# Optimization experiments

Hardware: AMD Instinct MI355X
Metric: run time of the kernel (lower is better)

## Reference

```python
import jax, jax.numpy as jnp
import numpy as np

DIM = 2048
DIM_HEAD = 128
HEADS = 16
FF_MULT = 4
EPS = 1e-05
ATTN_INNER = DIM_HEAD * HEADS          # 2048
FF_INNER = DIM * FF_MULT               # 8192
FUSED_DIMS = (ATTN_INNER, DIM_HEAD, DIM_HEAD, FF_INNER, FF_INNER)
SPLITS = np.cumsum(FUSED_DIMS[:-1]).tolist()
RMS_SCALE = DIM ** 0.5
Q_SCALE = DIM_HEAD ** (-0.5)


def setup_inputs() -> dict:
    key = jax.random.key(0)
    k1, k2, k3, k4, k5 = jax.random.split(key, 5)
    B, S = 2, 2048
    x = jax.random.normal(k1, (B, S, DIM), dtype=jnp.float32)
    attn_bias = jax.random.normal(k2, (HEADS, S, S), dtype=jnp.float32)
    # learned params (scaled for numerical sanity; math identical to module)
    gamma = jnp.ones((DIM,), dtype=jnp.float32)
    wi = jax.random.normal(k3, (DIM, sum(FUSED_DIMS)), dtype=jnp.float32) * 0.02
    attn_wo = jax.random.normal(k4, (ATTN_INNER, DIM), dtype=jnp.float32) * 0.02
    ff_wo = jax.random.normal(k5, (FF_INNER, DIM), dtype=jnp.float32) * 0.02
    return {"x": x, "attn_bias": attn_bias, "gamma": gamma,
            "wi": wi, "attn_wo": attn_wo, "ff_wo": ff_wo}


def reference(x, attn_bias, gamma, wi, attn_wo, ff_wo):
    B, S, _ = x.shape
    # RMSNorm
    inv_norm = jax.lax.rsqrt(jnp.sum(jnp.square(x), axis=-1, keepdims=True) + EPS)
    xn = inv_norm * x * gamma * RMS_SCALE
    # fused projection
    proj = xn @ wi  # [B, S, sum(fused_dims)]
    q, k, v, ff, ff_gate = jnp.split(proj, SPLITS, axis=-1)
    # q: [B, S, H*Dh] -> [B, H, S, Dh]; k, v stay single-head [B, S, Dh] (MQA)
    q = q.reshape(B, S, HEADS, DIM_HEAD).transpose(0, 2, 1, 3) * Q_SCALE
    sim = jnp.einsum('bhid,bjd->bhij', q, k) + attn_bias  # [B, H, S, S]
    attn = jax.nn.softmax(sim, axis=-1)
    out = jnp.einsum('bhij,bjd->bhid', attn, v)  # [B, H, S, Dh]
    out = out.transpose(0, 2, 1, 3).reshape(B, S, ATTN_INNER)
    attn_out = out @ attn_wo
    ff_out = (ff * jax.nn.swish(ff_gate)) @ ff_wo
    return attn_out + ff_out
```

## Files before the change

### kernel.cpp

```cpp
#include <hip/hip_runtime.h>
#include <cstdint>

typedef unsigned short u16;
typedef short bf16x8 __attribute__((ext_vector_type(8)));
typedef float f32x4 __attribute__((ext_vector_type(4)));

#define PLD 18688
#define ALD 10240
#define LOG2E 1.4426950408889634f
#define QSCALE 0.08838834764831845f
#define RMS_SCALE 45.25483399593904f

__device__ __forceinline__ u16 f2bf(float f) {
  union { float f; unsigned int u; } v; v.f = f;
  unsigned int u = v.u;
  return (u16)((u + 0x7fffu + ((u >> 16) & 1u)) >> 16);
}
__device__ __forceinline__ float bf2f(u16 h) {
  union { unsigned int u; float f; } v; v.u = ((unsigned int)h) << 16;
  return v.f;
}

__device__ __forceinline__ void gload_lds16(const void* g, void* l) {
  __builtin_amdgcn_global_load_lds((__attribute__((address_space(1))) void*)(g),
                                   (__attribute__((address_space(3))) void*)(l),
                                   16, 0, 0);
}

__global__ __launch_bounds__(256) void rmsnorm_kernel(const float* __restrict__ x,
                                                      const float* __restrict__ gamma,
                                                      u16* __restrict__ xn) {
  const int row = blockIdx.x;
  const int tid = threadIdx.x;
  const float4* xr = (const float4*)(x + (size_t)row * 2048);
  float4 v0 = xr[tid], v1 = xr[tid + 256];
  float s = v0.x*v0.x + v0.y*v0.y + v0.z*v0.z + v0.w*v0.w
          + v1.x*v1.x + v1.y*v1.y + v1.z*v1.z + v1.w*v1.w;
  for (int m = 1; m < 64; m <<= 1) s += __shfl_xor(s, m, 64);
  __shared__ float red[4];
  if ((tid & 63) == 0) red[tid >> 6] = s;
  __syncthreads();
  float tot = red[0] + red[1] + red[2] + red[3];
  float inv = rsqrtf(tot + 1e-5f) * RMS_SCALE;
  const float4* gp = (const float4*)gamma;
  float4 g0 = gp[tid], g1 = gp[tid + 256];
  u16* xo = xn + (size_t)row * 2048;
  union { u16 h[4]; uint2 u; } o0, o1;
  o0.h[0] = f2bf(v0.x*inv*g0.x); o0.h[1] = f2bf(v0.y*inv*g0.y);
  o0.h[2] = f2bf(v0.z*inv*g0.z); o0.h[3] = f2bf(v0.w*inv*g0.w);
  o1.h[0] = f2bf(v1.x*inv*g1.x); o1.h[1] = f2bf(v1.y*inv*g1.y);
  o1.h[2] = f2bf(v1.z*inv*g1.z); o1.h[3] = f2bf(v1.w*inv*g1.w);
  *(uint2*)(xo + tid*4) = o0.u;
  *(uint2*)(xo + (tid+256)*4) = o1.u;
}

__global__ __launch_bounds__(256) void tconv(const float* __restrict__ src,
                                             u16* __restrict__ dst,
                                             int K, int N, int dstride, int doff) {
  __shared__ u16 t[32][33];
  const int tx = threadIdx.x & 31, ty = threadIdx.x >> 5;
  const int n0 = blockIdx.x * 32, k0 = blockIdx.y * 32;
  #pragma unroll
  for (int yy = 0; yy < 4; yy++) {
    int r = ty + yy*8;
    t[r][tx] = f2bf(src[(size_t)(k0 + r) * N + n0 + tx]);
  }
  __syncthreads();
  #pragma unroll
  for (int yy = 0; yy < 4; yy++) {
    int r = ty + yy*8;
    dst[(size_t)(n0 + r) * dstride + doff + k0 + tx] = t[tx][r];
  }
}

template <int OUT_BF16, int GC>
__global__ __launch_bounds__(256) void gemm_bt(const u16* __restrict__ A,
                                               const u16* __restrict__ Bt,
                                               void* __restrict__ Cv,
                                               int M, int N, int K) {
  __shared__ alignas(16) u16 sA[128*32];
  __shared__ alignas(16) u16 sB[128*32];
  const int numRow = M >> 7;
  const int per = GC * numRow;
  const int pid = blockIdx.x;
  const int g = pid / per, inner = pid % per;
  const int colT = g * GC + inner / numRow;
  const int rowT = inner % numRow;
  const int row0 = rowT * 128, col0 = colT * 128;

  const int tid = threadIdx.x;
  const int w = tid >> 6, lane = tid & 63, quad = lane >> 4, l16 = lane & 15;
  const int wr = (w >> 1) * 64, wc = (w & 1) * 64;
  const f32x4 zero = {0.f, 0.f, 0.f, 0.f};
  f32x4 acc[4][4];
  #pragma unroll
  for (int mi = 0; mi < 4; mi++)
    #pragma unroll
    for (int ni = 0; ni < 4; ni++) acc[mi][ni] = zero;

  for (int k0 = 0; k0 < K; k0 += 32) {
    __syncthreads();
    #pragma unroll
    for (int i = 0; i < 2; i++) {
      const int segbase = (i*4 + w) * 64;
      const int seg = segbase + lane;
      const int r = seg >> 2, c = (seg & 3) * 8;
      gload_lds16(A  + (size_t)(row0 + r) * K + k0 + c, sA + segbase * 8);
      gload_lds16(Bt + (size_t)(col0 + r) * K + k0 + c, sB + segbase * 8);
    }
    __syncthreads();
    bf16x8 af[4], bfr[4];
    #pragma unroll
    for (int mi = 0; mi < 4; mi++)
      af[mi] = *(const bf16x8*)&sA[(wr + mi*16 + l16)*32 + quad*8];
    #pragma unroll
    for (int ni = 0; ni < 4; ni++)
      bfr[ni] = *(const bf16x8*)&sB[(wc + ni*16 + l16)*32 + quad*8];
    #pragma unroll
    for (int mi = 0; mi < 4; mi++)
      #pragma unroll
      for (int ni = 0; ni < 4; ni++)
        acc[mi][ni] = __builtin_amdgcn_mfma_f32_16x16x32_bf16(af[mi], bfr[ni], acc[mi][ni], 0, 0, 0);
  }

  #pragma unroll
  for (int mi = 0; mi < 4; mi++) {
    const int rb = row0 + wr + mi*16 + quad*4;
    #pragma unroll
    for (int ni = 0; ni < 4; ni++) {
      const int cb = col0 + wc + ni*16 + l16;
      #pragma unroll
      for (int r = 0; r < 4; r++) {
        if (OUT_BF16) ((u16*)Cv)[(size_t)(rb + r) * N + cb] = f2bf(acc[mi][ni][r]);
        else          ((float*)Cv)[(size_t)(rb + r) * N + cb] = acc[mi][ni][r];
      }
    }
  }
}

#define BAR() do { asm volatile("" ::: "memory"); __builtin_amdgcn_s_barrier(); asm volatile("" ::: "memory"); } while (0)
#define WAITV(N) asm volatile("s_waitcnt vmcnt(" #N ")" ::: "memory")

template <int OUT_BF16>
__global__ __launch_bounds__(512, 2) void gemm256(const u16* __restrict__ A,
                                                  const u16* __restrict__ Bt,
                                                  void* __restrict__ Cv,
                                                  int M, int N, int K) {
  __shared__ alignas(16) u16 lds[65536];
  u16* const sB = lds + 32768;

  const int numRow = M >> 8;
  int pid = blockIdx.x;
  {
    const int nwg = gridDim.x;
    const int q = nwg >> 3, r = nwg & 7;
    const int xcd = pid & 7, lid = pid >> 3;
    pid = (xcd < r ? xcd * (q + 1) : r * (q + 1) + (xcd - r) * q) + lid;
  }
  const int colT = pid / numRow, rowT = pid % numRow;
  const int row0 = rowT << 8, col0 = colT << 8;

  const int tid = threadIdx.x;
  const int w = tid >> 6, lane = tid & 63, quad = lane >> 4, l16 = lane & 15;
  const int wr = w >> 2, wc = w & 3;

  const u16* aG  = A  + (size_t)(row0 + w * 16 + l16) * K + quad * 8;
  const u16* aG2 = aG + (size_t)128 * K;
  const u16* bG  = Bt + (size_t)(col0 + w * 16 + l16) * K + quad * 8;
  const u16* bG2 = bG + (size_t)128 * K;

  #define STAGE_A(bb, ks, kt) do { \
    gload_lds16(aG  + (kt) + (ks) * 32, lds + (bb) * 16384 + (ks) * 8192 + w * 512); \
    gload_lds16(aG2 + (kt) + (ks) * 32, lds + (bb) * 16384 + (ks) * 8192 + (8 + w) * 512); \
  } while (0)
  #define STAGE_B(bb, ks, kt) do { \
    gload_lds16(bG  + (kt) + (ks) * 32, sB + (bb) * 16384 + (ks) * 8192 + w * 512); \
    gload_lds16(bG2 + (kt) + (ks) * 32, sB + (bb) * 16384 + (ks) * 8192 + (8 + w) * 512); \
  } while (0)

  const f32x4 zero = {0.f, 0.f, 0.f, 0.f};
  f32x4 acc[8][4];
  #pragma unroll
  for (int mi = 0; mi < 8; mi++)
    #pragma unroll
    for (int ni = 0; ni < 4; ni++) acc[mi][ni] = zero;

  const int nt = K >> 6;
  STAGE_A(0, 0, 0);  STAGE_B(0, 0, 0);
  STAGE_A(0, 1, 0);  STAGE_B(0, 1, 0);
  STAGE_A(1, 0, 64); STAGE_B(1, 0, 64);
  WAITV(8);
  BAR();

  const int aBase = wr * 8 * 512 + lane * 8;
  const int bBase = wc * 4 * 512 + lane * 8;

  for (int t = 0; t < nt; ++t) {
    const int bb = t & 1, nb = bb ^ 1;
    const int kt1 = (t + 1) << 6, kt2 = (t + 2) << 6;
    bf16x8 af[8], bf0, bf1;

    #pragma unroll
    for (int mi = 0; mi < 8; mi++)
      af[mi] = *(const bf16x8*)(lds + bb * 16384 + aBase + mi * 512);
    bf0 = *(const bf16x8*)(sB + bb * 16384 + bBase);
    bf1 = *(const bf16x8*)(sB + bb * 16384 + bBase + 512);
    if (t + 1 < nt) STAGE_A(nb, 1, kt1);
    BAR();
    __builtin_amdgcn_s_setprio(1);
    #pragma unroll
    for (int mi = 0; mi < 8; mi++) {
      acc[mi][0] = __builtin_amdgcn_mfma_f32_16x16x32_bf16(af[mi], bf0, acc[mi][0], 0, 0, 0);
      acc[mi][1] = __builtin_amdgcn_mfma_f32_16x16x32_bf16(af[mi], bf1, acc[mi][1], 0, 0, 0);
    }
    __builtin_amdgcn_s_setprio(0);
    BAR();

    bf0 = *(const bf16x8*)(sB + bb * 16384 + bBase + 1024);
    bf1 = *(const bf16x8*)(sB + bb * 16384 + bBase + 1536);
    if (t + 1 < nt) STAGE_B(nb, 1, kt1);
    BAR();
    __builtin_amdgcn_s_setprio(1);
    #pragma unroll
    for (int mi = 0; mi < 8; mi++) {
      acc[mi][2] = __builtin_amdgcn_mfma_f32_16x16x32_bf16(af[mi], bf0, acc[mi][2], 0, 0, 0);
      acc[mi][3] = __builtin_amdgcn_mfma_f32_16x16x32_bf16(af[mi], bf1, acc[mi][3], 0, 0, 0);
    }
    __builtin_amdgcn_s_setprio(0);
    if (t + 1 < nt) { WAITV(8); } else { WAITV(0); }
    BAR();

    #pragma unroll
    for (int mi = 0; mi < 8; mi++)
      af[mi] = *(const bf16x8*)(lds + bb * 16384 + 8192 + aBase + mi * 512);
    bf0 = *(const bf16x8*)(sB + bb * 16384 + 8192 + bBase);
    bf1 = *(const bf16x8*)(sB + bb * 16384 + 8192 + bBase + 512);
    if (t + 2 < nt) STAGE_A(bb, 0, kt2);
    BAR();
    __builtin_amdgcn_s_setprio(1);
    #pragma unroll
    for (int mi = 0; mi < 8; mi++) {
      acc[mi][0] = __builtin_amdgcn_mfma_f32_16x16x32_bf16(af[mi], bf0, acc[mi][0], 0, 0, 0);
      acc[mi][1] = __builtin_amdgcn_mfma_f32_16x16x32_bf16(af[mi], bf1, acc[mi][1], 0, 0, 0);
    }
    __builtin_amdgcn_s_setprio(0);
    BAR();

    bf0 = *(const bf16x8*)(sB + bb * 16384 + 8192 + bBase + 1024);
    bf1 = *(const bf16x8*)(sB + bb * 16384 + 8192 + bBase + 1536);
    if (t + 2 < nt) STAGE_B(bb, 0, kt2);
    BAR();
    __builtin_amdgcn_s_setprio(1);
    #pragma unroll
    for (int mi = 0; mi < 8; mi++) {
      acc[mi][2] = __builtin_amdgcn_mfma_f32_16x16x32_bf16(af[mi], bf0, acc[mi][2], 0, 0, 0);
      acc[mi][3] = __builtin_amdgcn_mfma_f32_16x16x32_bf16(af[mi], bf1, acc[mi][3], 0, 0, 0);
    }
    __builtin_amdgcn_s_setprio(0);
    if (t + 2 < nt)      { WAITV(8); }
    else if (t + 1 < nt) { WAITV(4); }
    BAR();
  }
  #undef STAGE_A
  #undef STAGE_B

  #pragma unroll
  for (int mi = 0; mi < 8; mi++) {
    const int rb = row0 + wr*128 + mi*16 + quad*4;
    #pragma unroll
    for (int ni = 0; ni < 4; ni++) {
      const int cb = col0 + wc*64 + ni*16 + l16;
      #pragma unroll
      for (int r = 0; r < 4; r++) {
        if (OUT_BF16) ((u16*)Cv)[(size_t)(rb + r) * N + cb] = f2bf(acc[mi][ni][r]);
        else          ((float*)Cv)[(size_t)(rb + r) * N + cb] = acc[mi][ni][r];
      }
    }
  }
}

__global__ __launch_bounds__(256) void ffh_kernel(const u16* __restrict__ proj,
                                                  u16* __restrict__ amat) {
  const int idx = blockIdx.x * 256 + threadIdx.x;
  const int row = idx >> 11;
  const int c = (idx & 2047) * 4;
  const u16* pr = proj + (size_t)row * PLD;
  uint2 fu = *(const uint2*)(pr + 2304 + c);
  uint2 gu = *(const uint2*)(pr + 10496 + c);
  u16 f[4] = {(u16)(fu.x & 0xffffu), (u16)(fu.x >> 16), (u16)(fu.y & 0xffffu), (u16)(fu.y >> 16)};
  u16 g[4] = {(u16)(gu.x & 0xffffu), (u16)(gu.x >> 16), (u16)(gu.y & 0xffffu), (u16)(gu.y >> 16)};
  union { u16 h[4]; uint2 u; } o;
  #pragma unroll
  for (int e = 0; e < 4; e++) {
    float gg = bf2f(g[e]);
    float sw = gg / (1.f + __expf(-gg));
    o.h[e] = f2bf(bf2f(f[e]) * sw);
  }
  *(uint2*)(amat + (size_t)row * ALD + 2048 + c) = o.u;
}

__global__ __launch_bounds__(256) void attn_kernel(const u16* __restrict__ proj,
                                                   const float* __restrict__ bias,
                                                   u16* __restrict__ amat) {
  const int it = blockIdx.x, h = blockIdx.y, b = blockIdx.z;
  const int tid = threadIdx.x;
  const int w = tid >> 6, lane = tid & 63, quad = lane >> 4, l16 = lane & 15;
  const int i0 = it * 64;
  __shared__ alignas(16) u16 kt[64*128];
  __shared__ alignas(16) u16 vt[128*64];
  __shared__ alignas(16) u16 pl[4][16*64];

  bf16x8 qf[4];
  {
    const u16* qp = proj + (size_t)(b*2048 + i0 + w*16 + l16) * PLD + h*128 + quad*8;
    #pragma unroll
    for (int kst = 0; kst < 4; kst++) qf[kst] = *(const bf16x8*)(qp + kst*32);
  }
  const f32x4 zero = {0.f, 0.f, 0.f, 0.f};
  f32x4 of[8];
  #pragma unroll
  for (int nd = 0; nd < 8; nd++) of[nd] = zero;
  float m_r[4] = {-1e30f, -1e30f, -1e30f, -1e30f};
  float l_r[4] = {0.f, 0.f, 0.f, 0.f};

  for (int j0 = 0; j0 < 2048; j0 += 64) {
    __syncthreads();
    #pragma unroll
    for (int i = 0; i < 4; i++) {
      const int segbase = (i*4 + w) * 64;
      const int seg = segbase + lane;
      const int r = seg >> 4;
      const int c16 = (seg & 15) ^ (r & 7);
      gload_lds16(proj + (size_t)(b*2048 + j0 + r) * PLD + 2048 + c16*8, kt + segbase*8);
    }
    #pragma unroll
    for (int e = 0; e < 16; e++) {
      const int flat = e*256 + tid;
      const int j = flat >> 6, d2 = (flat & 63) * 2;
      const unsigned int pv = *(const unsigned int*)(proj + (size_t)(b*2048 + j0 + j)*PLD + 2176 + d2);
      const int off = ((((j >> 3) ^ ((d2 >> 1) & 7)) << 3) + (j & 7));
      vt[d2*64 + off]     = (u16)(pv & 0xffffu);
      vt[(d2+1)*64 + off] = (u16)(pv >> 16);
    }
    __syncthreads();

    f32x4 sf[4];
    #pragma unroll
    for (int nj = 0; nj < 4; nj++) sf[nj] = zero;
    #pragma unroll
    for (int kst = 0; kst < 4; kst++)
      #pragma unroll
      for (int nj = 0; nj < 4; nj++) {
        bf16x8 bfr = *(const bf16x8*)&kt[(nj*16 + l16)*128 + (((kst*4 + quad) ^ (l16 & 7)))*8];
        sf[nj] = __builtin_amdgcn_mfma_f32_16x16x32_bf16(qf[kst], bfr, sf[nj], 0, 0, 0);
      }

    const float* bp = bias + ((size_t)h*2048 + (i0 + w*16 + quad*4)) * 2048 + j0 + l16;
    float s[4][4];
    #pragma unroll
    for (int nj = 0; nj < 4; nj++)
      #pragma unroll
      for (int r = 0; r < 4; r++)
        s[nj][r] = sf[nj][r] * QSCALE + bp[(size_t)r*2048 + nj*16];

    float p[4][4]; float alpha[4];
    #pragma unroll
    for (int r = 0; r < 4; r++) {
      float rm = fmaxf(fmaxf(s[0][r], s[1][r]), fmaxf(s[2][r], s[3][r]));
      rm = fmaxf(rm, __shfl_xor(rm, 1, 64));
      rm = fmaxf(rm, __shfl_xor(rm, 2, 64));
      rm = fmaxf(rm, __shfl_xor(rm, 4, 64));
      rm = fmaxf(rm, __shfl_xor(rm, 8, 64));
      const float mn = fmaxf(m_r[r], rm);
      alpha[r] = exp2f((m_r[r] - mn) * LOG2E);
      m_r[r] = mn;
      float rs = 0.f;
      #pragma unroll
      for (int nj = 0; nj < 4; nj++) { p[nj][r] = exp2f((s[nj][r] - mn) * LOG2E); rs += p[nj][r]; }
      rs += __shfl_xor(rs, 1, 64);
      rs += __shfl_xor(rs, 2, 64);
      rs += __shfl_xor(rs, 4, 64);
      rs += __shfl_xor(rs, 8, 64);
      l_r[r] = l_r[r] * alpha[r] + rs;
    }
    #pragma unroll
    for (int nd = 0; nd < 8; nd++)
      #pragma unroll
      for (int r = 0; r < 4; r++) of[nd][r] *= alpha[r];

    #pragma unroll
    for (int nj = 0; nj < 4; nj++)
      #pragma unroll
      for (int r = 0; r < 4; r++) {
        const int q = quad*4 + r;
        pl[w][q*64 + ((((nj*2 + (l16 >> 3)) ^ (q & 7)) << 3) + (l16 & 7))] = f2bf(p[nj][r]);
      }
    __syncthreads();

    #pragma unroll
    for (int k2 = 0; k2 < 2; k2++) {
      bf16x8 af = *(const bf16x8*)&pl[w][l16*64 + (((k2*4 + quad) ^ (l16 & 7)) << 3)];
      #pragma unroll
      for (int nd = 0; nd < 8; nd++) {
        bf16x8 bfr = *(const bf16x8*)&vt[(nd*16 + l16)*64 + (((k2*4 + quad) ^ (l16 >> 1)) << 3)];
        of[nd] = __builtin_amdgcn_mfma_f32_16x16x32_bf16(af, bfr, of[nd], 0, 0, 0);
      }
    }
  }

  const int token = b*2048 + i0 + w*16 + quad*4;
  #pragma unroll
  for (int r = 0; r < 4; r++) {
    const float invl = 1.f / l_r[r];
    u16* op = amat + (size_t)(token + r) * ALD + h*128 + l16;
    #pragma unroll
    for (int nd = 0; nd < 8; nd++) op[nd*16] = f2bf(of[nd][r] * invl);
  }
}

extern "C" void kernel_launch(void* const* d_in, const int* in_sizes, int n_in,
                              void* d_out, int out_size, void* d_ws, size_t ws_size,
                              hipStream_t stream) {
  const float* x       = (const float*)d_in[0];
  const float* bias    = (const float*)d_in[1];
  const float* gamma   = (const float*)d_in[2];
  const float* wi      = (const float*)d_in[3];
  const float* attn_wo = (const float*)d_in[4];
  const float* ff_wo   = (const float*)d_in[5];
  float* out = (float*)d_out;

  char* ws = (char*)d_ws;
  u16* xn   = (u16*)(ws);
  u16* wiT  = (u16*)(ws + 16777216);
  u16* amat = (u16*)(ws);
  u16* woT  = (u16*)(ws + 93323264);
  u16* proj = (u16*)(ws + 135266304);

  rmsnorm_kernel<<<4096, 256, 0, stream>>>(x, gamma, xn);
  tconv<<<dim3(18688/32, 2048/32), 256, 0, stream>>>(wi, wiT, 2048, 18688, 2048, 0);
  tconv<<<dim3(2048/32, 2048/32), 256, 0, stream>>>(attn_wo, woT, 2048, 2048, 10240, 0);
  tconv<<<dim3(2048/32, 8192/32), 256, 0, stream>>>(ff_wo, woT, 8192, 2048, 10240, 2048);
  gemm256<1><<<73*16, 512, 0, stream>>>(xn, wiT, proj, 4096, 18688, 2048);
  ffh_kernel<<<32768, 256, 0, stream>>>(proj, amat);
  attn_kernel<<<dim3(32, 16, 2), 256, 0, stream>>>(proj, bias, amat);
  gemm_bt<0, 16><<<16*32, 256, 0, stream>>>(amat, woT, out, 4096, 2048, 10240);
}
```

Before: 1.459 ms.

## Restructure GEMM inner loop into M-half quadrants with register-prefetched fragments

Splits each k-step's 8x4 MFMA block into four quadrants (top/bottom rows times k-sub-slice), loading the next quadrant's A/B fragments from LDS into registers while the current quadrant's MFMAs run, and prefetches the next tile's first fragments at the end of the iteration. The aim is to overlap LDS reads with matrix-core work and reduce the number of LDS B reads per step. Wait counts move to match the new stage order. The cost is higher register pressure from the extra fragment registers and more complex hazard reasoning between barriers and global-to-LDS stages.

```diff
diff --git a/kernel.cpp b/kernel.cpp
--- a/kernel.cpp
+++ b/kernel.cpp
@@ -186,79 +186,88 @@
     for (int ni = 0; ni < 4; ni++) acc[mi][ni] = zero;
 
   const int nt = K >> 6;
+  const int aBase = wr * 8 * 512 + lane * 8;
+  const int bBase = wc * 4 * 512 + lane * 8;
+
+  bf16x8 afX[4], afY[4], bfA[4], bfB[4];
+
   STAGE_A(0, 0, 0);  STAGE_B(0, 0, 0);
   STAGE_A(0, 1, 0);  STAGE_B(0, 1, 0);
   STAGE_A(1, 0, 64); STAGE_B(1, 0, 64);
   WAITV(8);
   BAR();
-
-  const int aBase = wr * 8 * 512 + lane * 8;
-  const int bBase = wc * 4 * 512 + lane * 8;
+  #pragma unroll
+  for (int i = 0; i < 4; i++) afX[i] = *(const bf16x8*)(lds + aBase + i * 512);
+  #pragma unroll
+  for (int i = 0; i < 4; i++) bfA[i] = *(const bf16x8*)(sB + bBase + i * 512);
 
   for (int t = 0; t < nt; ++t) {
     const int bb = t & 1, nb = bb ^ 1;
     const int kt1 = (t + 1) << 6, kt2 = (t + 2) << 6;
-    bf16x8 af[8], bf0, bf1;
-
-    #pragma unroll
-    for (int mi = 0; mi < 8; mi++)
-      af[mi] = *(const bf16x8*)(lds + bb * 16384 + aBase + mi * 512);
-    bf0 = *(const bf16x8*)(sB + bb * 16384 + bBase);
-    bf1 = *(const bf16x8*)(sB + bb * 16384 + bBase + 512);
+    const int A0 = bb * 16384 + aBase, A1 = A0 + 8192;
+    const int B0 = bb * 16384 + bBase, B1 = B0 + 8192;
+    const int nA0 = nb * 16384 + aBase;
+    const int nB0 = nb * 16384 + bBase;
+
+    #pragma unroll
+    for (int i = 0; i < 4; i++) afY[i] = *(const bf16x8*)(lds + A0 + (4 + i) * 512);
     if (t + 1 < nt) STAGE_A(nb, 1, kt1);
     BAR();
     __builtin_amdgcn_s_setprio(1);
     #pragma unroll
-    for (int mi = 0; mi < 8; mi++) {
-      acc[mi][0] = __builtin_amdgcn_mfma_f32_16x16x32_bf16(af[mi], bf0, acc[mi][0], 0, 0, 0);
-      acc[mi][1] = __builtin_amdgcn_mfma_f32_16x16x32_bf16(af[mi], bf1, acc[mi][1], 0, 0, 0);
-    }
+    for (int i = 0; i < 4; i++)
+      #pragma unroll
+      for (int ni = 0; ni < 4; ni++)
+        acc[i][ni] = __builtin_amdgcn_mfma_f32_16x16x32_bf16(afX[i], bfA[ni], acc[i][ni], 0, 0, 0);
     __builtin_amdgcn_s_setprio(0);
-    BAR();
-
-    bf0 = *(const bf16x8*)(sB + bb * 16384 + bBase + 1024);
-    bf1 = *(const bf16x8*)(sB + bb * 16384 + bBase + 1536);
+    if (t + 1 < nt) { WAITV(6); } else { WAITV(0); }
+    BAR();
+
+    #pragma unroll
+    for (int i = 0; i < 4; i++) afX[i] = *(const bf16x8*)(lds + A1 + i * 512);
+    #pragma unroll
+    for (int i = 0; i < 4; i++) bfB[i] = *(const bf16x8*)(sB + B1 + i * 512);
     if (t + 1 < nt) STAGE_B(nb, 1, kt1);
     BAR();
     __builtin_amdgcn_s_setprio(1);
     #pragma unroll
-    for (int mi = 0; mi < 8; mi++) {
-      acc[mi][2] = __builtin_amdgcn_mfma_f32_16x16x32_bf16(af[mi], bf0, acc[mi][2], 0, 0, 0);
-      acc[mi][3] = __builtin_amdgcn_mfma_f32_16x16x32_bf16(af[mi], bf1, acc[mi][3], 0, 0, 0);
-    }
+    for (int i = 0; i < 4; i++)
+      #pragma unroll
+      for (int ni = 0; ni < 4; ni++)
+        acc[4 + i][ni] = __builtin_amdgcn_mfma_f32_16x16x32_bf16(afY[i], bfA[ni], acc[4 + i][ni], 0, 0, 0);
     __builtin_amdgcn_s_setprio(0);
-    if (t + 1 < nt) { WAITV(8); } else { WAITV(0); }
-    BAR();
-
-    #pragma unroll
-    for (int mi = 0; mi < 8; mi++)
-      af[mi] = *(const bf16x8*)(lds + bb * 16384 + 8192 + aBase + mi * 512);
-    bf0 = *(const bf16x8*)(sB + bb * 16384 + 8192 + bBase);
-    bf1 = *(const bf16x8*)(sB + bb * 16384 + 8192 + bBase + 512);
+    BAR();
+
+    #pragma unroll
+    for (int i = 0; i < 4; i++) afY[i] = *(const bf16x8*)(lds + A1 + (4 + i) * 512);
     if (t + 2 < nt) STAGE_A(bb, 0, kt2);
     BAR();
     __builtin_amdgcn_s_setprio(1);
     #pragma unroll
-    for (int mi = 0; mi < 8; mi++) {
-      acc[mi][0] = __builtin_amdgcn_mfma_f32_16x16x32_bf16(af[mi], bf0, acc[mi][0], 0, 0, 0);
-      acc[mi][1] = __builtin_amdgcn_mfma_f32_16x16x32_bf16(af[mi], bf1, acc[mi][1], 0, 0, 0);
-    }
+    for (int i = 0; i < 4; i++)
+      #pragma unroll
+      for (int ni = 0; ni < 4; ni++)
+        acc[i][ni] = __builtin_amdgcn_mfma_f32_16x16x32_bf16(afX[i], bfB[ni], acc[i][ni], 0, 0, 0);
     __builtin_amdgcn_s_setprio(0);
-    BAR();
-
-    bf0 = *(const bf16x8*)(sB + bb * 16384 + 8192 + bBase + 1024);
-    bf1 = *(const bf16x8*)(sB + bb * 16384 + 8192 + bBase + 1536);
+    if (t + 2 < nt)      { WAITV(6); }
+    else if (t + 1 < nt) { WAITV(4); }
+    BAR();
+
+    if (t + 1 < nt) {
+      #pragma unroll
+      for (int i = 0; i < 4; i++) afX[i] = *(const bf16x8*)(lds + nA0 + i * 512);
+      #pragma unroll
+      for (int i = 0; i < 4; i++) bfA[i] = *(const bf16x8*)(sB + nB0 + i * 512);
+    }
     if (t + 2 < nt) STAGE_B(bb, 0, kt2);
     BAR();
     __builtin_amdgcn_s_setprio(1);
     #pragma unroll
-    for (int mi = 0; mi < 8; mi++) {
-      acc[mi][2] = __builtin_amdgcn_mfma_f32_16x16x32_bf16(af[mi], bf0, acc[mi][2], 0, 0, 0);
-      acc[mi][3] = __builtin_amdgcn_mfma_f32_16x16x32_bf16(af[mi], bf1, acc[mi][3], 0, 0, 0);
-    }
+    for (int i = 0; i < 4; i++)
+      #pragma unroll
+      for (int ni = 0; ni < 4; ni++)
+        acc[4 + i][ni] = __builtin_amdgcn_mfma_f32_16x16x32_bf16(afY[i], bfB[ni], acc[4 + i][ni], 0, 0, 0);
     __builtin_amdgcn_s_setprio(0);
-    if (t + 2 < nt)      { WAITV(8); }
-    else if (t + 1 < nt) { WAITV(4); }
     BAR();
   }
   #undef STAGE_A
```

Measured after the change: 1.458 ms. Within noise of the previous version (-0.0%).
